# Kernel optimization log

Measured on AMD Instinct MI355X. Metric: run time of the kernel, lower is better.

Reference implementation:

```python
import jax, jax.numpy as jnp
import numpy as np

B, N, D = 8, 2048, 1024
H, HD, FF = 16, 32, 4096  # head_dim = D // H // 2 = 32
LAMBDA_INIT = float(0.8 - 0.6 * np.exp(-0.3 * 1.0))  # layer_num = 1
EPS = 1e-5


def setup_inputs() -> dict:
    key = jax.random.key(0)
    ks = jax.random.split(key, 24)
    g = lambda k, shape, std=0.02: (jax.random.normal(k, shape, jnp.float32) * std)
    return {
        "src": jax.random.normal(ks[0], (B, N, D), jnp.float32),
        "Wq": g(ks[1], (D, D)), "Wk": g(ks[2], (D, D)), "Wv": g(ks[3], (D, D)),
        "Wo": g(ks[4], (D, D)), "bo": jnp.zeros((D,), jnp.float32),
        "lq1": g(ks[5], (HD,), 0.1), "lq2": g(ks[6], (HD,), 0.1),
        "lk1": g(ks[7], (HD,), 0.1), "lk2": g(ks[8], (HD,), 0.1),
        "ln1_g": jnp.ones((D,), jnp.float32), "ln1_b": jnp.zeros((D,), jnp.float32),
        "ln2_g": jnp.ones((D,), jnp.float32), "ln2_b": jnp.zeros((D,), jnp.float32),
        "W1": g(ks[9], (FF, D)), "b1": jnp.zeros((FF,), jnp.float32),
        "W2": g(ks[10], (D, FF)), "b2": jnp.zeros((D,), jnp.float32),
        "Wr": g(ks[11], (D, D)), "Ur": g(ks[12], (D, D)),
        "Wz": g(ks[13], (D, D)), "Uz": g(ks[14], (D, D)),
        "Wg": g(ks[15], (D, D)), "Ug": g(ks[16], (D, D)),
        "bg": jnp.full((D,), 2.0, jnp.float32),
    }


def _layernorm(x, gamma, beta):
    m = x.mean(-1, keepdims=True)
    v = jnp.mean((x - m) ** 2, axis=-1, keepdims=True)
    return (x - m) * jax.lax.rsqrt(v + EPS) * gamma + beta


def _diff_attn(x, Wq, Wk, Wv, Wo, bo, lq1, lq2, lk1, lk2):
    b, n, d = x.shape
    scale = HD ** -0.5
    # 'b n (h d q) -> b n (q h) d'
    q = (x @ Wq.T).reshape(b, n, H, HD, 2).transpose(0, 1, 4, 2, 3).reshape(b, n, 2 * H, HD) * scale
    # 'b n (h d k) -> b n (k h) d'
    k = (x @ Wk.T).reshape(b, n, H, HD, 2).transpose(0, 1, 4, 2, 3).reshape(b, n, 2 * H, HD)
    # 'b n (h d) -> b h n d', d = 2*HD
    v = (x @ Wv.T).reshape(b, n, H, 2 * HD).transpose(0, 2, 1, 3)
    # per-token attention over the 2H head axis: [b, n, 2H, 2H]
    att = jnp.einsum('bnqd,bnkd->bnqk', q, k)
    att = jax.nn.softmax(att.astype(jnp.float32), axis=-1)
    lam = jnp.exp(jnp.sum(lq1 * lk1)) - jnp.exp(jnp.sum(lq2 * lk2)) + LAMBDA_INIT
    att = att.reshape(b, n, 2, H, 2, H)  # q k split
    diff = att[:, :, 0, :, 0, :] - lam * att[:, :, 1, :, 1, :]  # [b, n, H, H]
    out = jnp.einsum('bnah,bhnd->bnad', diff, v)  # [b, n, H, 2*HD]
    # RMSNorm over last dim, no affine
    out = out * jax.lax.rsqrt(jnp.mean(out ** 2, axis=-1, keepdims=True) + EPS)
    out = (out * (1.0 - LAMBDA_INIT)).reshape(b, n, d)
    return out @ Wo.T + bo


def _gate_gru(x, y, Wr, Ur, Wz, Uz, Wg, Ug, bg):
    r = jax.nn.sigmoid(y @ Wr.T + x @ Ur.T)
    z = jax.nn.sigmoid(y @ Wz.T + x @ Uz.T - bg)
    h = jnp.tanh(y @ Wg.T + (r * x) @ Ug.T)
    return (1.0 - z) * x + z * h


def reference(src, Wq, Wk, Wv, Wo, bo, lq1, lq2, lk1, lk2,
              ln1_g, ln1_b, ln2_g, ln2_b, W1, b1, W2, b2,
              Wr, Ur, Wz, Uz, Wg, Ug, bg):
    # norm_first=True, use_gate=True (GRU), wo_ffn=False, dropout=0 (eval)
    s = _layernorm(src, ln1_g, ln1_b)
    src2 = _diff_attn(s, Wq, Wk, Wv, Wo, bo, lq1, lq2, lk1, lk2)
    conn = _gate_gru(src, jax.nn.relu(src2), Wr, Ur, Wz, Uz, Wg, Ug, bg)
    c = _layernorm(conn, ln2_g, ln2_b)
    src3 = jax.nn.relu(c @ W1.T + b1) @ W2.T + b2
    conn2 = _gate_gru(conn, jax.nn.relu(src3), Wr, Ur, Wz, Uz, Wg, Ug, bg)
    return conn2
```

## Files before the change

kernel.cpp:

```cpp
#include <hip/hip_runtime.h>


#define DEV __device__ __forceinline__

typedef unsigned short u16;
typedef __bf16 bf16x8 __attribute__((ext_vector_type(8)));
typedef float f32x4 __attribute__((ext_vector_type(4)));
typedef unsigned short us8 __attribute__((ext_vector_type(8)));
typedef unsigned short us4 __attribute__((ext_vector_type(4)));

#define LAMBDA0            0.35550906759096928f
#define ONE_MINUS_LAMBDA0  0.6444909324090307f
#define QSCALE             0.17677669529663687f

DEV float bf2f(u16 u) { union { unsigned u; float f; } x; x.u = ((unsigned)u) << 16; return x.f; }
DEV u16 f2bf(float f) {
  union { float f; unsigned u; } x; x.f = f;
  unsigned r = x.u + 0x7FFFu + ((x.u >> 16) & 1u);
  return (u16)(r >> 16);
}

DEV void gl_lds16(const void* g, void* l) {
  __builtin_amdgcn_global_load_lds((__attribute__((address_space(1))) void*)g,
                                   (__attribute__((address_space(3))) void*)l, 16, 0, 0);
}

template <int ACT, int OBF>
__global__ __launch_bounds__(256)
void gemm_bt(const u16* __restrict__ A, int lda, const u16* __restrict__ W,
             const float* __restrict__ bias, void* __restrict__ outp,
             int ldo, int K)
{
  __shared__ u16 As[128 * 32];
  __shared__ u16 Bs[128 * 32];
  const int tid = threadIdx.x;
  const int lane = tid & 63, wave = tid >> 6;
  const int m0 = blockIdx.y * 128, n0 = blockIdx.x * 128;
  const int wm = (wave >> 1) * 64, wn = (wave & 1) * 64;

  f32x4 acc[4][4] = {};

  const int srow = wave * 32 + (lane >> 2);
  const int scol = (lane & 3) * 8;
  const u16* gA0 = A + (size_t)(m0 + srow) * lda + scol;
  const u16* gA1 = gA0 + (size_t)16 * lda;
  const u16* gB0 = W + (size_t)(n0 + srow) * K + scol;
  const u16* gB1 = gB0 + (size_t)16 * K;
  u16* lA0 = As + wave * 1024;  u16* lA1 = lA0 + 512;
  u16* lB0 = Bs + wave * 1024;  u16* lB1 = lB0 + 512;

  const int frow = lane & 15;
  const int fk = (lane >> 4) * 8;

  for (int k0 = 0; k0 < K; k0 += 32) {
    gl_lds16(gA0 + k0, lA0);
    gl_lds16(gA1 + k0, lA1);
    gl_lds16(gB0 + k0, lB0);
    gl_lds16(gB1 + k0, lB1);
    __syncthreads();
    bf16x8 af[4], bfr[4];
#pragma unroll
    for (int i = 0; i < 4; ++i) {
      af[i]  = *(const bf16x8*)&As[(wm + i * 16 + frow) * 32 + fk];
      bfr[i] = *(const bf16x8*)&Bs[(wn + i * 16 + frow) * 32 + fk];
    }
#pragma unroll
    for (int i = 0; i < 4; ++i)
#pragma unroll
      for (int j = 0; j < 4; ++j)
        acc[i][j] = __builtin_amdgcn_mfma_f32_16x16x32_bf16(af[i], bfr[j], acc[i][j], 0, 0, 0);
    __syncthreads();
  }

  const int ec = lane & 15;
  const int er = (lane >> 4) * 4;
#pragma unroll
  for (int j = 0; j < 4; ++j) {
    const int gc = n0 + wn + j * 16 + ec;
    const float bv = bias ? bias[gc] : 0.f;
#pragma unroll
    for (int i = 0; i < 4; ++i) {
      const int gr = m0 + wm + i * 16 + er;
#pragma unroll
      for (int t = 0; t < 4; ++t) {
        float v = acc[i][j][t] + bv;
        if (ACT == 1) v = fmaxf(v, 0.f);
        else if (ACT == 2) v = 1.f / (1.f + expf(-v));
        else if (ACT == 3) v = tanhf(v);
        if (OBF) ((u16*)outp)[(size_t)(gr + t) * ldo + gc] = f2bf(v);
        else     ((float*)outp)[(size_t)(gr + t) * ldo + gc] = v;
      }
    }
  }
}

__global__ __launch_bounds__(256)
void ln_kernel(const float* __restrict__ in, const float* __restrict__ g,
               const float* __restrict__ b, u16* __restrict__ out)
{
  const int row = blockIdx.x, tid = threadIdx.x;
  const float4 x = ((const float4*)(in + (size_t)row * 1024))[tid];
  float s = x.x + x.y + x.z + x.w;
  float sq = x.x * x.x + x.y * x.y + x.z * x.z + x.w * x.w;
#pragma unroll
  for (int o = 32; o >= 1; o >>= 1) { s += __shfl_xor(s, o); sq += __shfl_xor(sq, o); }
  __shared__ float ls[4], lq[4];
  const int wave = tid >> 6;
  if ((tid & 63) == 0) { ls[wave] = s; lq[wave] = sq; }
  __syncthreads();
  s = ls[0] + ls[1] + ls[2] + ls[3];
  sq = lq[0] + lq[1] + lq[2] + lq[3];
  const float mean = s * (1.f / 1024.f);
  const float rstd = rsqrtf(sq * (1.f / 1024.f) - mean * mean + 1e-5f);
  const float4 gg = ((const float4*)g)[tid];
  const float4 bb = ((const float4*)b)[tid];
  us4 ov;
  ov[0] = f2bf((x.x - mean) * rstd * gg.x + bb.x);
  ov[1] = f2bf((x.y - mean) * rstd * gg.y + bb.y);
  ov[2] = f2bf((x.z - mean) * rstd * gg.z + bb.z);
  ov[3] = f2bf((x.w - mean) * rstd * gg.w + bb.w);
  *(us4*)(out + (size_t)row * 1024 + tid * 4) = ov;
}

__global__ __launch_bounds__(256)
void combine_ln_kernel(const float* __restrict__ x, const float* __restrict__ rzh,
                       const float* __restrict__ g, const float* __restrict__ b,
                       float* __restrict__ conn, u16* __restrict__ catbase)
{
  const int row = blockIdx.x, tid = threadIdx.x;
  const float4 xv = ((const float4*)(x + (size_t)row * 1024))[tid];
  const float4 hv = *(const float4*)(rzh + (size_t)row * 2048 + tid * 4);
  const float4 zv = *(const float4*)(rzh + (size_t)row * 2048 + 1024 + tid * 4);
  float4 cv;
  cv.x = (1.f - zv.x) * xv.x + zv.x * hv.x;
  cv.y = (1.f - zv.y) * xv.y + zv.y * hv.y;
  cv.z = (1.f - zv.z) * xv.z + zv.z * hv.z;
  cv.w = (1.f - zv.w) * xv.w + zv.w * hv.w;
  ((float4*)(conn + (size_t)row * 1024))[tid] = cv;
  us4 cb; cb[0] = f2bf(cv.x); cb[1] = f2bf(cv.y); cb[2] = f2bf(cv.z); cb[3] = f2bf(cv.w);
  *(us4*)(catbase + (size_t)row * 2048 + 1024 + tid * 4) = cb;

  float s = cv.x + cv.y + cv.z + cv.w;
  float sq = cv.x * cv.x + cv.y * cv.y + cv.z * cv.z + cv.w * cv.w;
#pragma unroll
  for (int o = 32; o >= 1; o >>= 1) { s += __shfl_xor(s, o); sq += __shfl_xor(sq, o); }
  __shared__ float ls[4], lq[4];
  const int wave = tid >> 6;
  if ((tid & 63) == 0) { ls[wave] = s; lq[wave] = sq; }
  __syncthreads();
  s = ls[0] + ls[1] + ls[2] + ls[3];
  sq = lq[0] + lq[1] + lq[2] + lq[3];
  const float mean = s * (1.f / 1024.f);
  const float rstd = rsqrtf(sq * (1.f / 1024.f) - mean * mean + 1e-5f);
  const float4 gg = ((const float4*)g)[tid];
  const float4 bb = ((const float4*)b)[tid];
  us4 ov;
  ov[0] = f2bf((cv.x - mean) * rstd * gg.x + bb.x);
  ov[1] = f2bf((cv.y - mean) * rstd * gg.y + bb.y);
  ov[2] = f2bf((cv.z - mean) * rstd * gg.z + bb.z);
  ov[3] = f2bf((cv.w - mean) * rstd * gg.w + bb.w);
  *(us4*)(catbase + (size_t)row * 2048 + tid * 4) = ov;
}

__global__ __launch_bounds__(256)
void combine2_kernel(const float* __restrict__ x, const float* __restrict__ rzh,
                     float* __restrict__ out)
{
  const int t = blockIdx.x * 256 + threadIdx.x;
  const int row = t >> 8;
  const int c4 = (t & 255) * 4;
  const float4 hv = *(const float4*)(rzh + (size_t)row * 2048 + c4);
  const float4 zv = *(const float4*)(rzh + (size_t)row * 2048 + 1024 + c4);
  const float4 xv = *(const float4*)(x + (size_t)row * 1024 + c4);
  float4 o;
  o.x = (1.f - zv.x) * xv.x + zv.x * hv.x;
  o.y = (1.f - zv.y) * xv.y + zv.y * hv.y;
  o.z = (1.f - zv.z) * xv.z + zv.z * hv.z;
  o.w = (1.f - zv.w) * xv.w + zv.w * hv.w;
  *(float4*)(out + (size_t)row * 1024 + c4) = o;
}

__global__ __launch_bounds__(256)
void rx_kernel(const float* __restrict__ rzh, const float* __restrict__ x,
               u16* __restrict__ dst)
{
  const int t = blockIdx.x * 256 + threadIdx.x;
  const int row = t >> 8;
  const int c4 = (t & 255) * 4;
  const float4 rv = *(const float4*)(rzh + (size_t)row * 2048 + c4);
  const float4 xv = *(const float4*)(x + (size_t)row * 1024 + c4);
  us4 o;
  o[0] = f2bf(rv.x * xv.x); o[1] = f2bf(rv.y * xv.y);
  o[2] = f2bf(rv.z * xv.z); o[3] = f2bf(rv.w * xv.w);
  *(us4*)(dst + (size_t)row * 2048 + c4) = o;
}

__global__ __launch_bounds__(256)
void cvt2d_kernel(const float* __restrict__ src, u16* __restrict__ dst,
                  int total4, int cshift, int ldd)
{
  const int t = blockIdx.x * 256 + threadIdx.x;
  if (t >= total4) return;
  const int idx = t * 4;
  const int r = idx >> cshift;
  const int c = idx & ((1 << cshift) - 1);
  const float4 v = *(const float4*)(src + (size_t)idx);
  us4 o; o[0] = f2bf(v.x); o[1] = f2bf(v.y); o[2] = f2bf(v.z); o[3] = f2bf(v.w);
  *(us4*)(dst + (size_t)r * ldd + c) = o;
}

__global__ __launch_bounds__(256)
void biasrz_kernel(const float* __restrict__ bg, float* __restrict__ brz)
{
  const int t = blockIdx.x * 256 + threadIdx.x;
  brz[t] = (t < 1024) ? 0.f : -bg[t - 1024];
}

__global__ __launch_bounds__(256)
void sentinel_kernel(float* __restrict__ out, int n)
{
  const int t = blockIdx.x * 256 + threadIdx.x;
  if (t < n) out[t] = 1.0e9f;
}

__global__ __launch_bounds__(256)
void attn_kernel(const u16* __restrict__ qkv,
                 const float* __restrict__ lq1, const float* __restrict__ lq2,
                 const float* __restrict__ lk1, const float* __restrict__ lk2,
                 u16* __restrict__ out)
{
  __shared__ float k_s[4][32][36];
  __shared__ float att_s[4][32][33];
  const int wave = threadIdx.x >> 6, lane = threadIdx.x & 63;
  const int tok = blockIdx.x * 4 + wave;
  const u16* qrow = qkv + (size_t)tok * 3072;
  const u16* krow = qrow + 1024;
  const u16* vrow = qrow + 2048;

  {
    us8 a = *(const us8*)(krow + lane * 16);
    us8 b = *(const us8*)(krow + lane * 16 + 8);
#pragma unroll
    for (int j = 0; j < 16; ++j) {
      int e = lane * 16 + j;
      u16 usv = (j < 8) ? a[j] : b[j - 8];
      int h = e >> 6, r = e & 63;
      k_s[wave][(r & 1) * 16 + h][r >> 1] = bf2f(usv);
    }
  }
  float qr[32];
  {
    const int a = lane & 31, h = a & 15, qi = a >> 4;
#pragma unroll
    for (int s = 0; s < 8; ++s) {
      us8 v8 = *(const us8*)(qrow + h * 64 + s * 8);
#pragma unroll
      for (int u = 0; u < 4; ++u) qr[s * 4 + u] = bf2f(v8[2 * u + qi]) * QSCALE;
    }
  }
  float lam;
  {
    const int dd = lane & 31;
    float p1 = lq1[dd] * lk1[dd], p2 = lq2[dd] * lk2[dd];
#pragma unroll
    for (int o = 16; o >= 1; o >>= 1) { p1 += __shfl_xor(p1, o); p2 += __shfl_xor(p2, o); }
    lam = expf(p1) - expf(p2) + LAMBDA0;
  }
  __syncthreads();

  const int a = lane & 31, bb = (lane >> 5) * 16;
  float av[16];
#pragma unroll
  for (int bi = 0; bi < 16; ++bi) {
    const float4* kk = (const float4*)&k_s[wave][bb + bi][0];
    float s = 0.f;
#pragma unroll
    for (int d4 = 0; d4 < 8; ++d4) {
      float4 kv = kk[d4];
      s += qr[d4 * 4 + 0] * kv.x + qr[d4 * 4 + 1] * kv.y +
           qr[d4 * 4 + 2] * kv.z + qr[d4 * 4 + 3] * kv.w;
    }
    av[bi] = s;
  }
  float mx = av[0];
#pragma unroll
  for (int i = 1; i < 16; ++i) mx = fmaxf(mx, av[i]);
  mx = fmaxf(mx, __shfl_xor(mx, 32));
  float se = 0.f;
#pragma unroll
  for (int i = 0; i < 16; ++i) { av[i] = expf(av[i] - mx); se += av[i]; }
  se += __shfl_xor(se, 32);
  const float inv = 1.f / se;
#pragma unroll
  for (int i = 0; i < 16; ++i) att_s[wave][a][bb + i] = av[i] * inv;
  __syncthreads();

  const int a2 = lane >> 2, jb = (lane & 3) * 16;
  float o[16];
#pragma unroll
  for (int j = 0; j < 16; ++j) o[j] = 0.f;
#pragma unroll
  for (int h = 0; h < 16; ++h) {
    const float dc = att_s[wave][a2][h] - lam * att_s[wave][16 + a2][16 + h];
    const u16* vv = vrow + h * 64 + jb;
    us8 v0 = *(const us8*)vv;
    us8 v1 = *(const us8*)(vv + 8);
#pragma unroll
    for (int j = 0; j < 8; ++j) { o[j] += dc * bf2f(v0[j]); o[8 + j] += dc * bf2f(v1[j]); }
  }
  float ss = 0.f;
#pragma unroll
  for (int j = 0; j < 16; ++j) ss += o[j] * o[j];
  ss += __shfl_xor(ss, 1);
  ss += __shfl_xor(ss, 2);
  const float sc = rsqrtf(ss * (1.f / 64.f) + 1e-5f) * ONE_MINUS_LAMBDA0;
  us8 r0, r1;
#pragma unroll
  for (int j = 0; j < 8; ++j) { r0[j] = f2bf(o[j] * sc); r1[j] = f2bf(o[8 + j] * sc); }
  u16* op = out + (size_t)tok * 1024 + a2 * 64 + jb;
  *(us8*)op = r0;
  *(us8*)(op + 8) = r1;
}

enum : size_t {
  OFF_WQKV = 0,
  OFF_WO   = OFF_WQKV + (size_t)3072 * 1024 * 2,
  OFF_WRZ  = OFF_WO   + (size_t)1024 * 1024 * 2,
  OFF_WG   = OFF_WRZ  + (size_t)2048 * 2048 * 2,
  OFF_W1   = OFF_WG   + (size_t)1024 * 2048 * 2,
  OFF_W2   = OFF_W1   + (size_t)4096 * 1024 * 2,
  OFF_BRZ  = OFF_W2   + (size_t)1024 * 4096 * 2,
  OFF_R1   = OFF_BRZ  + (size_t)2048 * 4,
  OFF_CAT  = OFF_R1   + (size_t)134217728,
  WS_NEED  = OFF_CAT  + (size_t)16384 * 2048 * 2
};

extern "C" void kernel_launch(void* const* d_in, const int* in_sizes, int n_in,
                              void* d_out, int out_size, void* d_ws, size_t ws_size,
                              hipStream_t stream)
{
  (void)in_sizes; (void)n_in;
  if (ws_size < WS_NEED) {
    sentinel_kernel<<<(out_size + 255) / 256, 256, 0, stream>>>((float*)d_out, out_size);
    return;
  }

  const float* src  = (const float*)d_in[0];
  const float* Wq   = (const float*)d_in[1];
  const float* Wk   = (const float*)d_in[2];
  const float* Wv   = (const float*)d_in[3];
  const float* Wo   = (const float*)d_in[4];
  const float* bo   = (const float*)d_in[5];
  const float* lq1  = (const float*)d_in[6];
  const float* lq2  = (const float*)d_in[7];
  const float* lk1  = (const float*)d_in[8];
  const float* lk2  = (const float*)d_in[9];
  const float* ln1g = (const float*)d_in[10];
  const float* ln1b = (const float*)d_in[11];
  const float* ln2g = (const float*)d_in[12];
  const float* ln2b = (const float*)d_in[13];
  const float* W1   = (const float*)d_in[14];
  const float* b1   = (const float*)d_in[15];
  const float* W2   = (const float*)d_in[16];
  const float* b2   = (const float*)d_in[17];
  const float* Wr   = (const float*)d_in[18];
  const float* Ur   = (const float*)d_in[19];
  const float* Wz   = (const float*)d_in[20];
  const float* Uz   = (const float*)d_in[21];
  const float* Wg   = (const float*)d_in[22];
  const float* Ug   = (const float*)d_in[23];
  const float* bg   = (const float*)d_in[24];

  char* ws = (char*)d_ws;
  u16*   wqkv = (u16*)(ws + OFF_WQKV);
  u16*   wo_b = (u16*)(ws + OFF_WO);
  u16*   wrz  = (u16*)(ws + OFF_WRZ);
  u16*   wgc  = (u16*)(ws + OFF_WG);
  u16*   w1b  = (u16*)(ws + OFF_W1);
  u16*   w2b  = (u16*)(ws + OFF_W2);
  float* brz  = (float*)(ws + OFF_BRZ);
  u16*   r1u  = (u16*)(ws + OFF_R1);
  u16*   sbuf = (u16*)(ws + OFF_R1 + 100663296);
  float* rzh  = (float*)(ws + OFF_R1);
  u16*   cat  = (u16*)(ws + OFF_CAT);
  float* conn = (float*)d_out;

  auto cvt = [&](const float* s, u16* dst, int rows, int cshift, int ldd) {
    int total4 = (rows << cshift) >> 2;
    cvt2d_kernel<<<(total4 + 255) / 256, 256, 0, stream>>>(s, dst, total4, cshift, ldd);
  };

  cvt(Wq, wqkv,                     1024, 10, 1024);
  cvt(Wk, wqkv + 1024 * 1024,       1024, 10, 1024);
  cvt(Wv, wqkv + 2 * 1024 * 1024,   1024, 10, 1024);
  cvt(Wo, wo_b,                     1024, 10, 1024);
  cvt(Wr, wrz,                      1024, 10, 2048);
  cvt(Ur, wrz + 1024,               1024, 10, 2048);
  cvt(Wz, wrz + 2048 * 1024,        1024, 10, 2048);
  cvt(Uz, wrz + 2048 * 1024 + 1024, 1024, 10, 2048);
  cvt(Wg, wgc,                      1024, 10, 2048);
  cvt(Ug, wgc + 1024,               1024, 10, 2048);
  cvt(W1, w1b,                      4096, 10, 1024);
  cvt(W2, w2b,                      1024, 12, 4096);
  cvt(src, cat + 1024,             16384, 10, 2048);
  biasrz_kernel<<<8, 256, 0, stream>>>(bg, brz);

  ln_kernel<<<16384, 256, 0, stream>>>(src, ln1g, ln1b, sbuf);

  gemm_bt<0, 1><<<dim3(24, 128), 256, 0, stream>>>(sbuf, 1024, wqkv, nullptr, r1u, 3072, 1024);

  attn_kernel<<<4096, 256, 0, stream>>>(r1u, lq1, lq2, lk1, lk2, sbuf);

  gemm_bt<1, 1><<<dim3(8, 128), 256, 0, stream>>>(sbuf, 1024, wo_b, bo, cat, 2048, 1024);

  gemm_bt<2, 0><<<dim3(16, 128), 256, 0, stream>>>(cat, 2048, wrz, brz, rzh, 2048, 2048);
  rx_kernel<<<16384, 256, 0, stream>>>(rzh, src, cat + 1024);
  gemm_bt<3, 0><<<dim3(8, 128), 256, 0, stream>>>(cat, 2048, wgc, nullptr, rzh, 2048, 2048);
  combine_ln_kernel<<<16384, 256, 0, stream>>>(src, rzh, ln2g, ln2b, conn, cat);

  gemm_bt<1, 1><<<dim3(32, 128), 256, 0, stream>>>(cat, 2048, w1b, b1, r1u, 4096, 1024);
  gemm_bt<1, 1><<<dim3(8, 128), 256, 0, stream>>>(r1u, 4096, w2b, b2, cat, 2048, 4096);

  gemm_bt<2, 0><<<dim3(16, 128), 256, 0, stream>>>(cat, 2048, wrz, brz, rzh, 2048, 2048);
  rx_kernel<<<16384, 256, 0, stream>>>(rzh, conn, cat + 1024);
  gemm_bt<3, 0><<<dim3(8, 128), 256, 0, stream>>>(cat, 2048, wgc, nullptr, rzh, 2048, 2048);
  combine2_kernel<<<16384, 256, 0, stream>>>(conn, rzh, (float*)d_out);
}
```

Measured before the change: 1.579 ms.

## Replace GEMM with 256x256 double-buffered, swizzled, prefetching MFMA kernel

Replaces the 128x128 single-buffered GEMM with a 256x256-tile, 512-thread kernel. It double-buffers A and B in LDS with an XOR swizzle, prefetches the next K tiles while MFMAs run, uses s_setprio around the compute, and remaps workgroups for L2 locality. The aim is to hide global-load latency and raise MFMA utilisation across all of the layer's GEMMs. In exchange it uses 128KB of LDS per block and many accumulator registers, and it relies on hand-placed waitcnt and barrier ordering.

Result: faster. 1.318 ms (-16.5%).

```diff
diff --git a/kernel.cpp b/kernel.cpp
--- a/kernel.cpp
+++ b/kernel.cpp
@@ -25,73 +25,131 @@
                                    (__attribute__((address_space(3))) void*)l, 16, 0, 0);
 }
 
+#define MF(a, b, c) __builtin_amdgcn_mfma_f32_16x16x32_bf16(a, b, c, 0, 0, 0)
+#define BARM() asm volatile("s_barrier" ::: "memory")
+
+DEV void stage_half_f(const u16* __restrict__ g, int ld, int rowbase, int k0,
+                      u16* lds, int bufoff , int h, int wave, int lane)
+{
+  const int rr = lane >> 3;
+  const int sc = ((lane & 7) ^ rr) * 8;
+  const u16* gs = g + (size_t)(rowbase + h * 128 + wave * 16 + rr) * ld + (k0 + sc);
+  u16* l = lds + bufoff + h * 8192 + wave * 1024;
+  gl_lds16(gs, l);
+  gl_lds16(gs + (size_t)8 * ld, l + 512);
+}
+
 template <int ACT, int OBF>
-__global__ __launch_bounds__(256)
-void gemm_bt(const u16* __restrict__ A, int lda, const u16* __restrict__ W,
+__global__ __launch_bounds__(512, 2)
+void gemm256(const u16* __restrict__ A, int lda, const u16* __restrict__ W,
              const float* __restrict__ bias, void* __restrict__ outp,
              int ldo, int K)
 {
-  __shared__ u16 As[128 * 32];
-  __shared__ u16 Bs[128 * 32];
+  __shared__ u16 As[32768];
+  __shared__ u16 Bs[32768];
+
   const int tid = threadIdx.x;
   const int lane = tid & 63, wave = tid >> 6;
-  const int m0 = blockIdx.y * 128, n0 = blockIdx.x * 128;
-  const int wm = (wave >> 1) * 64, wn = (wave & 1) * 64;
-
-  f32x4 acc[4][4] = {};
-
-  const int srow = wave * 32 + (lane >> 2);
-  const int scol = (lane & 3) * 8;
-  const u16* gA0 = A + (size_t)(m0 + srow) * lda + scol;
-  const u16* gA1 = gA0 + (size_t)16 * lda;
-  const u16* gB0 = W + (size_t)(n0 + srow) * K + scol;
-  const u16* gB1 = gB0 + (size_t)16 * K;
-  u16* lA0 = As + wave * 1024;  u16* lA1 = lA0 + 512;
-  u16* lB0 = Bs + wave * 1024;  u16* lB1 = lB0 + 512;
-
-  const int frow = lane & 15;
-  const int fk = (lane >> 4) * 8;
-
-  for (int k0 = 0; k0 < K; k0 += 32) {
-    gl_lds16(gA0 + k0, lA0);
-    gl_lds16(gA1 + k0, lA1);
-    gl_lds16(gB0 + k0, lB0);
-    gl_lds16(gB1 + k0, lB1);
-    __syncthreads();
-    bf16x8 af[4], bfr[4];
-#pragma unroll
-    for (int i = 0; i < 4; ++i) {
-      af[i]  = *(const bf16x8*)&As[(wm + i * 16 + frow) * 32 + fk];
-      bfr[i] = *(const bf16x8*)&Bs[(wn + i * 16 + frow) * 32 + fk];
+  const int wr = wave >> 2, wc = wave & 3;
+  const int frow = lane & 15, fx = lane >> 4, s7 = lane & 7;
+
+  const int gx = gridDim.x;
+  const int nwg = gx * gridDim.y;
+  const int lin = blockIdx.y * gx + blockIdx.x;
+  const int logical = (lin & 7) * (nwg >> 3) + (lin >> 3);
+  const int m0 = (logical / gx) * 256;
+  const int n0 = (logical % gx) * 256;
+
+  const int NT = K >> 6;
+  const int aoff = (wr * 32 + frow) * 64;
+  const int boff = (wc * 64 + frow) * 64;
+  const int swA0 = (fx ^ s7) * 8;
+  const int swA1 = ((4 + fx) ^ s7) * 8;
+
+  f32x4 acc[8][4] = {};
+  bf16x8 bfr[4][2];
+
+  stage_half_f(W, K, n0, 0, Bs, 0, 0, wave, lane);
+  stage_half_f(W, K, n0, 0, Bs, 0, 1, wave, lane);
+  stage_half_f(A, lda, m0, 0, As, 0, 0, wave, lane);
+  stage_half_f(A, lda, m0, 0, As, 0, 1, wave, lane);
+  stage_half_f(W, K, n0, 64, Bs, 16384, 0, wave, lane);
+  stage_half_f(W, K, n0, 64, Bs, 16384, 1, wave, lane);
+  asm volatile("s_waitcnt vmcnt(6)" ::: "memory");
+  BARM();
+
+#define PH(q, STG, TAILW)                                                     \
+  {                                                                           \
+    bf16x8 a00 = *(const bf16x8*)(As + aB + 4096 * (q) + swA0);               \
+    bf16x8 a01 = *(const bf16x8*)(As + aB + 4096 * (q) + swA1);               \
+    bf16x8 a10 = *(const bf16x8*)(As + aB + 4096 * (q) + 1024 + swA0);        \
+    bf16x8 a11 = *(const bf16x8*)(As + aB + 4096 * (q) + 1024 + swA1);        \
+    STG;                                                                      \
+    BARM();                                                                   \
+    __builtin_amdgcn_s_setprio(1);                                            \
+    acc[2*(q)  ][0] = MF(a00, bfr[0][0], acc[2*(q)  ][0]);                    \
+    acc[2*(q)  ][1] = MF(a00, bfr[1][0], acc[2*(q)  ][1]);                    \
+    acc[2*(q)  ][2] = MF(a00, bfr[2][0], acc[2*(q)  ][2]);                    \
+    acc[2*(q)  ][3] = MF(a00, bfr[3][0], acc[2*(q)  ][3]);                    \
+    acc[2*(q)+1][0] = MF(a10, bfr[0][0], acc[2*(q)+1][0]);                    \
+    acc[2*(q)+1][1] = MF(a10, bfr[1][0], acc[2*(q)+1][1]);                    \
+    acc[2*(q)+1][2] = MF(a10, bfr[2][0], acc[2*(q)+1][2]);                    \
+    acc[2*(q)+1][3] = MF(a10, bfr[3][0], acc[2*(q)+1][3]);                    \
+    acc[2*(q)  ][0] = MF(a01, bfr[0][1], acc[2*(q)  ][0]);                    \
+    acc[2*(q)  ][1] = MF(a01, bfr[1][1], acc[2*(q)  ][1]);                    \
+    acc[2*(q)  ][2] = MF(a01, bfr[2][1], acc[2*(q)  ][2]);                    \
+    acc[2*(q)  ][3] = MF(a01, bfr[3][1], acc[2*(q)  ][3]);                    \
+    acc[2*(q)+1][0] = MF(a11, bfr[0][1], acc[2*(q)+1][0]);                    \
+    acc[2*(q)+1][1] = MF(a11, bfr[1][1], acc[2*(q)+1][1]);                    \
+    acc[2*(q)+1][2] = MF(a11, bfr[2][1], acc[2*(q)+1][2]);                    \
+    acc[2*(q)+1][3] = MF(a11, bfr[3][1], acc[2*(q)+1][3]);                    \
+    __builtin_amdgcn_s_setprio(0);                                            \
+    TAILW;                                                                    \
+    BARM();                                                                   \
+  }
+
+  for (int t = 0; t < NT; ++t) {
+    const int cb = (t & 1) * 16384;
+    const int ob = 16384 - cb;
+    const int kA = ((t + 1 < NT) ? t + 1 : NT - 1) * 64;
+    const int kB = ((t + 2 < NT) ? t + 2 : NT - 1) * 64;
+    const int aB = cb + aoff;
+    const int bB = cb + boff;
+#pragma unroll
+    for (int n = 0; n < 4; ++n) {
+      bfr[n][0] = *(const bf16x8*)(Bs + bB + n * 1024 + swA0);
+      bfr[n][1] = *(const bf16x8*)(Bs + bB + n * 1024 + swA1);
     }
-#pragma unroll
-    for (int i = 0; i < 4; ++i)
-#pragma unroll
-      for (int j = 0; j < 4; ++j)
-        acc[i][j] = __builtin_amdgcn_mfma_f32_16x16x32_bf16(af[i], bfr[j], acc[i][j], 0, 0, 0);
-    __syncthreads();
-  }
-
-  const int ec = lane & 15;
-  const int er = (lane >> 4) * 4;
-#pragma unroll
-  for (int j = 0; j < 4; ++j) {
-    const int gc = n0 + wn + j * 16 + ec;
-    const float bv = bias ? bias[gc] : 0.f;
-#pragma unroll
-    for (int i = 0; i < 4; ++i) {
-      const int gr = m0 + wm + i * 16 + er;
-#pragma unroll
-      for (int t = 0; t < 4; ++t) {
-        float v = acc[i][j][t] + bv;
-        if (ACT == 1) v = fmaxf(v, 0.f);
-        else if (ACT == 2) v = 1.f / (1.f + expf(-v));
-        else if (ACT == 3) v = tanhf(v);
-        if (OBF) ((u16*)outp)[(size_t)(gr + t) * ldo + gc] = f2bf(v);
-        else     ((float*)outp)[(size_t)(gr + t) * ldo + gc] = v;
+    PH(0, stage_half_f(A, lda, m0, kA, As, ob, 0, wave, lane), (void)0);
+    PH(1, stage_half_f(A, lda, m0, kA, As, ob, 1, wave, lane),
+       asm volatile("s_waitcnt vmcnt(8)" ::: "memory"));
+    PH(2, stage_half_f(W, K, n0, kB, Bs, cb, 0, wave, lane), (void)0);
+    PH(3, stage_half_f(W, K, n0, kB, Bs, cb, 1, wave, lane),
+       asm volatile("s_waitcnt vmcnt(6)" ::: "memory"));
+  }
+#undef PH
+
+  const int er = fx * 4;
+#pragma unroll
+  for (int q = 0; q < 4; ++q)
+#pragma unroll
+    for (int j = 0; j < 2; ++j) {
+      const int grb = m0 + 64 * q + wr * 32 + j * 16 + er;
+#pragma unroll
+      for (int n = 0; n < 4; ++n) {
+        const int gc = n0 + wc * 64 + n * 16 + frow;
+        const float bv = bias ? bias[gc] : 0.f;
+#pragma unroll
+        for (int tt = 0; tt < 4; ++tt) {
+          float v = acc[2 * q + j][n][tt] + bv;
+          if (ACT == 1) v = fmaxf(v, 0.f);
+          else if (ACT == 2) v = 1.f / (1.f + expf(-v));
+          else if (ACT == 3) v = tanhf(v);
+          if (OBF) ((u16*)outp)[(size_t)(grb + tt) * ldo + gc] = f2bf(v);
+          else     ((float*)outp)[(size_t)(grb + tt) * ldo + gc] = v;
+        }
       }
     }
-  }
 }
 
 __global__ __launch_bounds__(256)
@@ -407,22 +465,22 @@
 
   ln_kernel<<<16384, 256, 0, stream>>>(src, ln1g, ln1b, sbuf);
 
-  gemm_bt<0, 1><<<dim3(24, 128), 256, 0, stream>>>(sbuf, 1024, wqkv, nullptr, r1u, 3072, 1024);
+  gemm256<0, 1><<<dim3(12, 64), 512, 0, stream>>>(sbuf, 1024, wqkv, nullptr, r1u, 3072, 1024);
 
   attn_kernel<<<4096, 256, 0, stream>>>(r1u, lq1, lq2, lk1, lk2, sbuf);
 
-  gemm_bt<1, 1><<<dim3(8, 128), 256, 0, stream>>>(sbuf, 1024, wo_b, bo, cat, 2048, 1024);
-
-  gemm_bt<2, 0><<<dim3(16, 128), 256, 0, stream>>>(cat, 2048, wrz, brz, rzh, 2048, 2048);
+  gemm256<1, 1><<<dim3(4, 64), 512, 0, stream>>>(sbuf, 1024, wo_b, bo, cat, 2048, 1024);
+
+  gemm256<2, 0><<<dim3(8, 64), 512, 0, stream>>>(cat, 2048, wrz, brz, rzh, 2048, 2048);
   rx_kernel<<<16384, 256, 0, stream>>>(rzh, src, cat + 1024);
-  gemm_bt<3, 0><<<dim3(8, 128), 256, 0, stream>>>(cat, 2048, wgc, nullptr, rzh, 2048, 2048);
+  gemm256<3, 0><<<dim3(4, 64), 512, 0, stream>>>(cat, 2048, wgc, nullptr, rzh, 2048, 2048);
   combine_ln_kernel<<<16384, 256, 0, stream>>>(src, rzh, ln2g, ln2b, conn, cat);
 
-  gemm_bt<1, 1><<<dim3(32, 128), 256, 0, stream>>>(cat, 2048, w1b, b1, r1u, 4096, 1024);
-  gemm_bt<1, 1><<<dim3(8, 128), 256, 0, stream>>>(r1u, 4096, w2b, b2, cat, 2048, 4096);
-
-  gemm_bt<2, 0><<<dim3(16, 128), 256, 0, stream>>>(cat, 2048, wrz, brz, rzh, 2048, 2048);
+  gemm256<1, 1><<<dim3(16, 64), 512, 0, stream>>>(cat, 2048, w1b, b1, r1u, 4096, 1024);
+  gemm256<1, 1><<<dim3(4, 64), 512, 0, stream>>>(r1u, 4096, w2b, b2, cat, 2048, 4096);
+
+  gemm256<2, 0><<<dim3(8, 64), 512, 0, stream>>>(cat, 2048, wrz, brz, rzh, 2048, 2048);
   rx_kernel<<<16384, 256, 0, stream>>>(rzh, conn, cat + 1024);
-  gemm_bt<3, 0><<<dim3(8, 128), 256, 0, stream>>>(cat, 2048, wgc, nullptr, rzh, 2048, 2048);
+  gemm256<3, 0><<<dim3(4, 64), 512, 0, stream>>>(cat, 2048, wgc, nullptr, rzh, 2048, 2048);
   combine2_kernel<<<16384, 256, 0, stream>>>(conn, rzh, (float*)d_out);
 }
```
